# Kernel optimization log

Hardware: AMD Instinct MI355X
Metric: run time of the kernel (lower is better)

Reference implementation:

```python
import jax, jax.numpy as jnp
import numpy as np

B, L, D_IN, D_MODEL, H = 8, 1024, 256, 512, 8
D_HEAD = D_MODEL // H


def setup_inputs() -> dict:
    key = jax.random.key(0)
    ks = jax.random.split(key, 12)
    queries = jax.random.normal(ks[0], (B, L, D_IN), dtype=jnp.float32)
    keys_ = jax.random.normal(ks[1], (B, L, D_IN), dtype=jnp.float32)
    values = jax.random.normal(ks[2], (B, L, D_IN), dtype=jnp.float32)
    attention_mask = jnp.ones((B, L), dtype=jnp.int32)
    # binary symmetric-ish adjacency (sparse molecular graph style)
    adjacency_matrix = (jax.random.uniform(ks[3], (B, L, L)) < 0.05).astype(jnp.float32)
    distance_matrix = jax.random.uniform(ks[4], (B, L, L), dtype=jnp.float32) * 10.0
    s = 1.0 / np.sqrt(D_IN)
    W_q = jax.random.normal(ks[5], (D_MODEL, D_IN), dtype=jnp.float32) * s
    W_k = jax.random.normal(ks[6], (D_MODEL, D_IN), dtype=jnp.float32) * s
    W_v = jax.random.normal(ks[7], (D_MODEL, D_IN), dtype=jnp.float32) * s
    W_o = jax.random.normal(ks[8], (D_MODEL, D_MODEL), dtype=jnp.float32) / np.sqrt(D_MODEL)
    lambda_a = jax.random.normal(ks[9], (H,), dtype=jnp.float32) * 0.1
    lambda_d = jax.random.normal(ks[10], (H,), dtype=jnp.float32) * 0.1
    return {"queries": queries, "keys": keys_, "values": values,
            "attention_mask": attention_mask, "adjacency_matrix": adjacency_matrix,
            "distance_matrix": distance_matrix, "W_q": W_q, "W_k": W_k,
            "W_v": W_v, "W_o": W_o, "lambda_a": lambda_a, "lambda_d": lambda_d}


def _split_heads(x):
    # (b, l, d_model) -> (b, h, l, d_head)
    b, l, _ = x.shape
    return x.reshape(b, l, H, D_HEAD).transpose(0, 2, 1, 3)


def reference(queries, keys, values, attention_mask, adjacency_matrix,
              distance_matrix, W_q, W_k, W_v, W_o, lambda_a, lambda_d):
    Q = _split_heads(queries @ W_q.T)   # (b,h,l,d)
    K = _split_heads(keys @ W_k.T)
    V = _split_heads(values @ W_v.T)
    scores = jnp.einsum("bhqd,bhkd->bhqk", Q, K) / jnp.sqrt(jnp.asarray(D_HEAD, Q.dtype))
    # MSRSA: per-head learned scalars inject graph structure into the scores
    scores = (scores
              + lambda_a[None, :, None, None] * adjacency_matrix[:, None, :, :]
              + lambda_d[None, :, None, None] * distance_matrix[:, None, :, :])
    mask = attention_mask[:, None, None, :] > 0  # (b,1,1,l) key mask
    scores = jnp.where(mask, scores, jnp.asarray(-1e9, scores.dtype))
    attn_weight = jax.nn.softmax(scores, axis=-1)  # (b,h,l,l)
    out = jnp.einsum("bhqk,bhkd->bhqd", attn_weight, V)
    out = out.transpose(0, 2, 1, 3).reshape(queries.shape[0], queries.shape[1], D_MODEL)
    return out @ W_o.T
```

## Files before the change

kernel.cpp:

```cpp
#include <hip/hip_runtime.h>
#include <hip/hip_fp16.h>

#define BB 8
#define LL 1024
#define DIN 256
#define DM 512
#define HH 8
#define DH 64

typedef __attribute__((ext_vector_type(8))) short bf16x8;
typedef __attribute__((ext_vector_type(4))) float f32x4;

__device__ __forceinline__ unsigned short f2bf(float f) {
  union { float f; unsigned u; } c; c.f = f;
  unsigned u = c.u;
  return (unsigned short)((u + 0x7fffu + ((u >> 16) & 1u)) >> 16);
}

#if defined(__has_builtin)
#if __has_builtin(__builtin_amdgcn_cvt_pk_bf16_f32)
#define HAS_PK_BF16 1
#endif
#if __has_builtin(__builtin_amdgcn_fdot2)
#define HAS_FDOT2 1
#endif
#endif

#ifdef HAS_PK_BF16
typedef __bf16 bf2 __attribute__((ext_vector_type(2)));
__device__ __forceinline__ unsigned pk2(float lo, float hi) {
  union { bf2 v; unsigned u; } c;
  c.v = __builtin_amdgcn_cvt_pk_bf16_f32(lo, hi);
  return c.u;
}
#else
__device__ __forceinline__ unsigned pk2(float lo, float hi) {
  return ((unsigned)f2bf(hi) << 16) | f2bf(lo);
}
#endif

typedef _Float16 h2f __attribute__((ext_vector_type(2)));

__device__ __forceinline__ unsigned pkh(float a, float d) {
  return (unsigned)__half_as_ushort(__float2half_rn(a)) |
         ((unsigned)__half_as_ushort(__float2half_rn(d)) << 16);
}

__device__ __forceinline__ void async_copy16(void* lds, const void* g) {
  __builtin_amdgcn_global_load_lds(
      (const __attribute__((address_space(1))) unsigned*)g,
      (__attribute__((address_space(3))) unsigned*)lds, 16, 0, 0);
}

__global__ __launch_bounds__(256) void prep(
    const float* __restrict__ qin, const float* __restrict__ kin,
    const float* __restrict__ vin,
    const float* __restrict__ wq, const float* __restrict__ wk,
    const float* __restrict__ wv, const float* __restrict__ wo,
    const int* __restrict__ msk,
    const float* __restrict__ adj, const float* __restrict__ dis,
    unsigned short* __restrict__ xq, unsigned short* __restrict__ xk,
    unsigned short* __restrict__ xv,
    unsigned short* __restrict__ wqb, unsigned short* __restrict__ wkb,
    unsigned short* __restrict__ wvb, unsigned short* __restrict__ wob,
    float* __restrict__ mad, unsigned* __restrict__ bp)
{
  int t = blockIdx.x * 256 + threadIdx.x;
  const int XS = 524288, WS = 32768;
  if (t < 3 * XS) {
    int seg = t >> 19, off = t & (XS - 1);
    const float* s = (seg == 0) ? qin : (seg == 1) ? kin : vin;
    unsigned short* d = (seg == 0) ? xq : (seg == 1) ? xk : xv;
    float4 f = ((const float4*)s)[off];
    uint2 o = { pk2(f.x, f.y), pk2(f.z, f.w) };
    ((uint2*)d)[off] = o;
    return;
  }
  t -= 3 * XS;
  if (t < 3 * WS) {
    int seg = t >> 15, off = t & (WS - 1);
    const float* s = (seg == 0) ? wq : (seg == 1) ? wk : wv;
    unsigned short* d = (seg == 0) ? wqb : (seg == 1) ? wkb : wvb;
    float4 f = ((const float4*)s)[off];
    uint2 o = { pk2(f.x, f.y), pk2(f.z, f.w) };
    ((uint2*)d)[off] = o;
    return;
  }
  t -= 3 * WS;
  if (t < 65536) {
    float4 f = ((const float4*)wo)[t];
    uint2 o = { pk2(f.x, f.y), pk2(f.z, f.w) };
    ((uint2*)wob)[t] = o;
    return;
  }
  t -= 65536;
  if (t < 2048) {
    int4 m = ((const int4*)msk)[t];
    float4 f = { m.x ? 0.0f : -30000.0f, m.y ? 0.0f : -30000.0f,
                 m.z ? 0.0f : -30000.0f, m.w ? 0.0f : -30000.0f };
    ((float4*)mad)[t] = f;
    return;
  }
  t -= 2048;
  float4 a4 = ((const float4*)adj)[t];
  float4 d4 = ((const float4*)dis)[t];
  uint4 o = { pkh(a4.x, d4.x), pkh(a4.y, d4.y), pkh(a4.z, d4.z), pkh(a4.w, d4.w) };
  ((uint4*)bp)[t] = o;
}

__global__ __launch_bounds__(256) void qkv_proj(
    const unsigned short* __restrict__ xq, const unsigned short* __restrict__ xk,
    const unsigned short* __restrict__ xv,
    const unsigned short* __restrict__ wqb, const unsigned short* __restrict__ wkb,
    const unsigned short* __restrict__ wvb,
    unsigned short* __restrict__ qb, unsigned short* __restrict__ kb,
    unsigned short* __restrict__ vt)
{
  const int t = blockIdx.z;
  const unsigned short* __restrict__ X = (t == 0) ? xq : (t == 1) ? xk : xv;
  const unsigned short* __restrict__ W = (t == 0) ? wqb : (t == 1) ? wkb : wvb;
  const int m0 = blockIdx.y * 128;
  const int h  = blockIdx.x;
  __shared__ __align__(16) char arena[24576];
  const int tid = threadIdx.x;
  const int wid = tid >> 6;
  const int lane = tid & 63;
  const int lo = lane & 15;
  const int quad = lane >> 4;

  f32x4 acc[2][4];
#pragma unroll
  for (int mi = 0; mi < 2; ++mi)
#pragma unroll
    for (int ni = 0; ni < 4; ++ni) acc[mi][ni] = (f32x4)0.0f;

#pragma unroll
  for (int j = 0; j < 2; ++j) {
    int id = j * 256 + tid, r = id >> 2, c = id & 3;
    async_copy16(arena + j * 4096 + wid * 1024,
                 X + (size_t)(m0 + r) * DIN + ((c ^ (r & 3)) * 8));
  }
  {
    int id = tid, r = id >> 2, c = id & 3;
    async_copy16(arena + 16384 + wid * 1024,
                 W + (size_t)(h * 64 + r) * DIN + ((c ^ (r & 3)) * 8));
  }
  __syncthreads();

  for (int it = 0; it < 8; ++it) {
    const int p = it & 1;
    if (it < 7) {
      const int kk = (it + 1) * 32, q = 1 - p;
#pragma unroll
      for (int j = 0; j < 2; ++j) {
        int id = j * 256 + tid, r = id >> 2, c = id & 3;
        async_copy16(arena + q * 8192 + j * 4096 + wid * 1024,
                     X + (size_t)(m0 + r) * DIN + kk + ((c ^ (r & 3)) * 8));
      }
      {
        int id = tid, r = id >> 2, c = id & 3;
        async_copy16(arena + 16384 + q * 4096 + wid * 1024,
                     W + (size_t)(h * 64 + r) * DIN + kk + ((c ^ (r & 3)) * 8));
      }
    }
    const unsigned short* Ab = (const unsigned short*)(arena + p * 8192);
    const unsigned short* Bb = (const unsigned short*)(arena + 16384 + p * 4096);
    bf16x8 a[2], bfr[4];
#pragma unroll
    for (int mi = 0; mi < 2; ++mi) {
      int R = wid * 32 + mi * 16 + lo;
      a[mi] = *(const bf16x8*)&Ab[R * 32 + ((quad ^ (R & 3)) * 8)];
    }
#pragma unroll
    for (int ni = 0; ni < 4; ++ni) {
      int N = ni * 16 + lo;
      bfr[ni] = *(const bf16x8*)&Bb[N * 32 + ((quad ^ (N & 3)) * 8)];
    }
#pragma unroll
    for (int mi = 0; mi < 2; ++mi)
#pragma unroll
      for (int ni = 0; ni < 4; ++ni)
        acc[mi][ni] = __builtin_amdgcn_mfma_f32_16x16x32_bf16(
            a[mi], bfr[ni], acc[mi][ni], 0, 0, 0);
    __syncthreads();
  }

  const int b = m0 >> 10;
  const int lbase0 = (m0 & 1023) + wid * 32;
  if (t < 2) {
    unsigned short* dstp = (t == 0) ? qb : kb;
#pragma unroll
    for (int mi = 0; mi < 2; ++mi)
#pragma unroll
      for (int ni = 0; ni < 4; ++ni) {
        int d = ni * 16 + lo;
#pragma unroll
        for (int r = 0; r < 4; ++r) {
          int lb = lbase0 + mi * 16 + quad * 4 + r;
          dstp[((size_t)(b * HH + h) * LL + lb) * DH + d] = f2bf(acc[mi][ni][r]);
        }
      }
  } else {
#pragma unroll
    for (int mi = 0; mi < 2; ++mi)
#pragma unroll
      for (int ni = 0; ni < 4; ++ni) {
        int d = ni * 16 + lo;
        int lb = lbase0 + mi * 16 + quad * 4;
        uint2 o = { pk2(acc[mi][ni][0], acc[mi][ni][1]),
                    pk2(acc[mi][ni][2], acc[mi][ni][3]) };
        *(uint2*)&vt[((size_t)(b * HH + h) * DH + d) * LL + lb] = o;
      }
  }
}

__global__ __launch_bounds__(256, 4) void attn(
    const unsigned short* __restrict__ qb, const unsigned short* __restrict__ kb,
    const unsigned short* __restrict__ vt,
    const float* __restrict__ mad, const unsigned* __restrict__ bp,
    const float* __restrict__ la_, const float* __restrict__ ld_,
    unsigned short* __restrict__ ao)
{
  const int bi = blockIdx.x;
  const int b  = bi & 7;
  const int hg = (bi >> 3) & 3;
  const int q0 = (bi >> 5) * 32;
  const int tid = threadIdx.x;
  const int wid = tid >> 6;
  const int lane = tid & 63;
  const int lo = lane & 15;
  const int quad = lane >> 4;
  const int h  = hg * 2 + (wid & 1);
  const int kh = wid >> 1;
  const int bh = b * HH + h;

  __shared__ __align__(16) char arena[17408];
  unsigned short* pbufw = (unsigned short*)arena + wid * 1280;
  float*          mgbuf = (float*)arena;

  const float LOG2E = 1.44269504f;
  const float la2 = la_[h] * LOG2E, ld2 = ld_[h] * LOG2E;
  const float sc2 = 0.125f * LOG2E;
#ifdef HAS_FDOT2
  h2f lam2;
  lam2.x = (_Float16)la2;
  lam2.y = (_Float16)ld2;
#endif

  const unsigned short* qp = qb + ((size_t)bh * LL + q0) * DH;
  bf16x8 qB[2][2];
#pragma unroll
  for (int nj = 0; nj < 2; ++nj)
#pragma unroll
    for (int ki = 0; ki < 2; ++ki)
      qB[nj][ki] = *(const bf16x8*)&qp[(nj * 16 + lo) * DH + ki * 32 + quad * 8];

  const unsigned short* kp = kb + (size_t)bh * LL * DH;
  const unsigned short* vp = vt + (size_t)bh * DH * LL;
  const unsigned* bpp = bp + ((size_t)b * LL + q0) * LL;
  const float* mp = mad + b * LL;

  f32x4 o[4][2];
  float rs[2] = {0.0f, 0.0f};
#pragma unroll
  for (int md = 0; md < 4; ++md)
#pragma unroll
    for (int nj = 0; nj < 2; ++nj) o[md][nj] = (f32x4)0.0f;

  const int kbeg = kh * (LL / 2);

  for (int jt = 0; jt < 16; ++jt) {
    const int k0 = kbeg + jt * 32;

    bf16x8 kA[2][2];
#pragma unroll
    for (int mi = 0; mi < 2; ++mi)
#pragma unroll
      for (int ki = 0; ki < 2; ++ki)
        kA[mi][ki] = *(const bf16x8*)&kp[(size_t)(k0 + mi * 16 + lo) * DH +
                                         ki * 32 + quad * 8];
    bf16x8 vA[4];
#pragma unroll
    for (int md = 0; md < 4; ++md)
      vA[md] = *(const bf16x8*)&vp[(md * 16 + lo) * LL + k0 + quad * 8];
    f32x4 msv[2];
#pragma unroll
    for (int mi = 0; mi < 2; ++mi)
      msv[mi] = *(const f32x4*)&mp[k0 + mi * 16 + quad * 4];

    f32x4 s[2][2];
#pragma unroll
    for (int mi = 0; mi < 2; ++mi)
#pragma unroll
      for (int nj = 0; nj < 2; ++nj) s[mi][nj] = (f32x4)0.0f;
#pragma unroll
    for (int ki = 0; ki < 2; ++ki)
#pragma unroll
      for (int mi = 0; mi < 2; ++mi)
#pragma unroll
        for (int nj = 0; nj < 2; ++nj)
          s[mi][nj] = __builtin_amdgcn_mfma_f32_16x16x32_bf16(
              kA[mi][ki], qB[nj][ki], s[mi][nj], 0, 0, 0);

#pragma unroll
    for (int mi = 0; mi < 2; ++mi)
#pragma unroll
      for (int nj = 0; nj < 2; ++nj) {
        uint4 u = *(const uint4*)&bpp[(size_t)(nj * 16 + lo) * LL +
                                      k0 + mi * 16 + quad * 4];
        float p4[4];
#pragma unroll
        for (int r = 0; r < 4; ++r) {
          float t = fmaf(s[mi][nj][r], sc2, msv[mi][r]);
#ifdef HAS_FDOT2
          union { unsigned v; h2f hv; } c; c.v = u[r];
          p4[r] = __builtin_amdgcn_exp2f(
              __builtin_amdgcn_fdot2(c.hv, lam2, t, false));
#else
          union { unsigned v; __half2 hh; } c; c.v = u[r];
          float tt = fmaf(__high2float(c.hh), ld2, t);
          p4[r] = __builtin_amdgcn_exp2f(fmaf(__low2float(c.hh), la2, tt));
#endif
        }
        rs[nj] += (p4[0] + p4[1]) + (p4[2] + p4[3]);
        uint2 w = { pk2(p4[0], p4[1]), pk2(p4[2], p4[3]) };
        *(uint2*)&pbufw[(nj * 16 + lo) * 40 + mi * 16 + quad * 4] = w;
      }

    asm volatile("s_waitcnt lgkmcnt(0)" ::: "memory");

    bf16x8 pB[2];
#pragma unroll
    for (int nj = 0; nj < 2; ++nj)
      pB[nj] = *(const bf16x8*)&pbufw[(nj * 16 + lo) * 40 + quad * 8];

#pragma unroll
    for (int md = 0; md < 4; ++md)
#pragma unroll
      for (int nj = 0; nj < 2; ++nj)
        o[md][nj] = __builtin_amdgcn_mfma_f32_16x16x32_bf16(
            vA[md], pB[nj], o[md][nj], 0, 0, 0);
  }

  __syncthreads();
  const int hs = wid & 1;
  if (kh == 1) {
#pragma unroll
    for (int md = 0; md < 4; ++md)
#pragma unroll
      for (int nj = 0; nj < 2; ++nj)
#pragma unroll
        for (int r = 0; r < 4; ++r)
          mgbuf[hs * 2176 + ((md * 2 + nj) * 4 + r) * 64 + lane] = o[md][nj][r];
    mgbuf[hs * 2176 + 32 * 64 + lane] = rs[0];
    mgbuf[hs * 2176 + 33 * 64 + lane] = rs[1];
  }
  __syncthreads();
  if (kh == 0) {
#pragma unroll
    for (int md = 0; md < 4; ++md)
#pragma unroll
      for (int nj = 0; nj < 2; ++nj)
#pragma unroll
        for (int r = 0; r < 4; ++r)
          o[md][nj][r] += mgbuf[hs * 2176 + ((md * 2 + nj) * 4 + r) * 64 + lane];
    rs[0] += mgbuf[hs * 2176 + 32 * 64 + lane];
    rs[1] += mgbuf[hs * 2176 + 33 * 64 + lane];
    float inv[2];
#pragma unroll
    for (int nj = 0; nj < 2; ++nj) {
      rs[nj] += __shfl_xor(rs[nj], 16);
      rs[nj] += __shfl_xor(rs[nj], 32);
      inv[nj] = __builtin_amdgcn_rcpf(rs[nj]);
    }
#pragma unroll
    for (int md = 0; md < 4; ++md)
#pragma unroll
      for (int nj = 0; nj < 2; ++nj) {
        int l = q0 + nj * 16 + lo;
        uint2 st = { pk2(o[md][nj][0] * inv[nj], o[md][nj][1] * inv[nj]),
                     pk2(o[md][nj][2] * inv[nj], o[md][nj][3] * inv[nj]) };
        *(uint2*)&ao[((size_t)b * LL + l) * DM + h * DH + md * 16 + quad * 4] = st;
      }
  }
}

__global__ __launch_bounds__(256) void oproj(
    const unsigned short* __restrict__ ao, const unsigned short* __restrict__ wob,
    float* __restrict__ out)
{
  const int m0 = blockIdx.y * 128;
  const int n0 = blockIdx.x * 64;
  __shared__ __align__(16) char arena[24576];
  const int tid = threadIdx.x;
  const int wid = tid >> 6;
  const int lane = tid & 63;
  const int lo = lane & 15;
  const int quad = lane >> 4;

  f32x4 acc[2][4];
#pragma unroll
  for (int mi = 0; mi < 2; ++mi)
#pragma unroll
    for (int ni = 0; ni < 4; ++ni) acc[mi][ni] = (f32x4)0.0f;

#pragma unroll
  for (int j = 0; j < 2; ++j) {
    int id = j * 256 + tid, r = id >> 2, c = id & 3;
    async_copy16(arena + j * 4096 + wid * 1024,
                 ao + (size_t)(m0 + r) * DM + ((c ^ (r & 3)) * 8));
  }
  {
    int id = tid, r = id >> 2, c = id & 3;
    async_copy16(arena + 16384 + wid * 1024,
                 wob + (size_t)(n0 + r) * DM + ((c ^ (r & 3)) * 8));
  }
  __syncthreads();

  for (int it = 0; it < 16; ++it) {
    const int p = it & 1;
    if (it < 15) {
      const int kk = (it + 1) * 32, q = 1 - p;
#pragma unroll
      for (int j = 0; j < 2; ++j) {
        int id = j * 256 + tid, r = id >> 2, c = id & 3;
        async_copy16(arena + q * 8192 + j * 4096 + wid * 1024,
                     ao + (size_t)(m0 + r) * DM + kk + ((c ^ (r & 3)) * 8));
      }
      {
        int id = tid, r = id >> 2, c = id & 3;
        async_copy16(arena + 16384 + q * 4096 + wid * 1024,
                     wob + (size_t)(n0 + r) * DM + kk + ((c ^ (r & 3)) * 8));
      }
    }
    const unsigned short* Ab = (const unsigned short*)(arena + p * 8192);
    const unsigned short* Bb = (const unsigned short*)(arena + 16384 + p * 4096);
    bf16x8 a[2], bfr[4];
#pragma unroll
    for (int mi = 0; mi < 2; ++mi) {
      int R = wid * 32 + mi * 16 + lo;
      a[mi] = *(const bf16x8*)&Ab[R * 32 + ((quad ^ (R & 3)) * 8)];
    }
#pragma unroll
    for (int ni = 0; ni < 4; ++ni) {
      int N = ni * 16 + lo;
      bfr[ni] = *(const bf16x8*)&Bb[N * 32 + ((quad ^ (N & 3)) * 8)];
    }
#pragma unroll
    for (int mi = 0; mi < 2; ++mi)
#pragma unroll
      for (int ni = 0; ni < 4; ++ni)
        acc[mi][ni] = __builtin_amdgcn_mfma_f32_16x16x32_bf16(
            a[mi], bfr[ni], acc[mi][ni], 0, 0, 0);
    __syncthreads();
  }

#pragma unroll
  for (int mi = 0; mi < 2; ++mi)
#pragma unroll
    for (int ni = 0; ni < 4; ++ni)
#pragma unroll
      for (int r = 0; r < 4; ++r)
        out[(size_t)(m0 + wid * 32 + mi * 16 + quad * 4 + r) * DM +
            n0 + ni * 16 + lo] = acc[mi][ni][r];
}

extern "C" void kernel_launch(void* const* d_in, const int* in_sizes, int n_in,
                              void* d_out, int out_size, void* d_ws, size_t ws_size,
                              hipStream_t stream) {
  const float* qin = (const float*)d_in[0];
  const float* kin = (const float*)d_in[1];
  const float* vin = (const float*)d_in[2];
  const int*   msk = (const int*)d_in[3];
  const float* adj = (const float*)d_in[4];
  const float* dis = (const float*)d_in[5];
  const float* wq  = (const float*)d_in[6];
  const float* wk  = (const float*)d_in[7];
  const float* wv  = (const float*)d_in[8];
  const float* wo  = (const float*)d_in[9];
  const float* la  = (const float*)d_in[10];
  const float* ld  = (const float*)d_in[11];
  float* out = (float*)d_out;

  const size_t tensb = (size_t)BB * HH * LL * DH;
  const size_t xsz   = (size_t)BB * LL * DIN;
  unsigned short* qb  = (unsigned short*)d_ws;
  unsigned short* kb  = qb + tensb;
  unsigned short* vt  = kb + tensb;
  unsigned short* ao  = vt + tensb;
  unsigned short* xq  = ao;
  unsigned short* xk  = ao + xsz;
  unsigned short* xv  = ao + tensb;
  unsigned short* wqb = xv + xsz;
  unsigned short* wkb = wqb + (size_t)DM * DIN;
  unsigned short* wvb = wkb + (size_t)DM * DIN;
  unsigned short* wob = wvb + (size_t)DM * DIN;
  float*          mdd = (float*)(wob + (size_t)DM * DM);
  unsigned*       bpk = (unsigned*)(mdd + (size_t)BB * LL);

  prep<<<dim3(14984), 256, 0, stream>>>(qin, kin, vin, wq, wk, wv, wo, msk,
                                        adj, dis,
                                        xq, xk, xv, wqb, wkb, wvb, wob, mdd, bpk);
  qkv_proj<<<dim3(8, 64, 3), 256, 0, stream>>>(xq, xk, xv, wqb, wkb, wvb, qb, kb, vt);
  attn<<<dim3(1024), 256, 0, stream>>>(qb, kb, vt, mdd, bpk, la, ld, ao);
  oproj<<<dim3(8, 64), 256, 0, stream>>>(ao, wob, out);
}
```

Baseline: 270.8 us.

## Prefetch next K tile and issue bias loads before score MFMAs in attention loop

Restructures the attention inner loop into a manually double-buffered pair of tiles. The K fragment for the next tile is loaded while the current tile computes, and the packed adjacency/distance bias, mask and V loads are issued up front behind a sched_barrier, so global latency overlaps the score MFMAs. The launch-bounds occupancy hint drops from 4 to 3 blocks to leave room for the extra registers, and the fdot2 bias path becomes unconditional on device. The risks are higher register pressure and lower occupancy.

```diff
diff --git a/kernel.cpp b/kernel.cpp
--- a/kernel.cpp
+++ b/kernel.cpp
@@ -10,6 +10,7 @@
 
 typedef __attribute__((ext_vector_type(8))) short bf16x8;
 typedef __attribute__((ext_vector_type(4))) float f32x4;
+typedef _Float16 h2f __attribute__((ext_vector_type(2)));
 
 __device__ __forceinline__ unsigned short f2bf(float f) {
   union { float f; unsigned u; } c; c.f = f;
@@ -21,12 +22,9 @@
 #if __has_builtin(__builtin_amdgcn_cvt_pk_bf16_f32)
 #define HAS_PK_BF16 1
 #endif
-#if __has_builtin(__builtin_amdgcn_fdot2)
-#define HAS_FDOT2 1
 #endif
-#endif
-
-#ifdef HAS_PK_BF16
+
+#if defined(HAS_PK_BF16)
 typedef __bf16 bf2 __attribute__((ext_vector_type(2)));
 __device__ __forceinline__ unsigned pk2(float lo, float hi) {
   union { bf2 v; unsigned u; } c;
@@ -39,7 +37,15 @@
 }
 #endif
 
-typedef _Float16 h2f __attribute__((ext_vector_type(2)));
+__device__ __forceinline__ float biasdot(unsigned u, h2f lam, float t) {
+#if defined(__HIP_DEVICE_COMPILE__)
+  union { unsigned v; h2f hv; } c; c.v = u;
+  return __builtin_amdgcn_fdot2(c.hv, lam, t, false);
+#else
+  (void)u; (void)lam;
+  return t;
+#endif
+}
 
 __device__ __forceinline__ unsigned pkh(float a, float d) {
   return (unsigned)__half_as_ushort(__float2half_rn(a)) |
@@ -214,7 +220,7 @@
   }
 }
 
-__global__ __launch_bounds__(256, 4) void attn(
+__global__ __launch_bounds__(256, 3) void attn(
     const unsigned short* __restrict__ qb, const unsigned short* __restrict__ kb,
     const unsigned short* __restrict__ vt,
     const float* __restrict__ mad, const unsigned* __restrict__ bp,
@@ -241,11 +247,9 @@
   const float LOG2E = 1.44269504f;
   const float la2 = la_[h] * LOG2E, ld2 = ld_[h] * LOG2E;
   const float sc2 = 0.125f * LOG2E;
-#ifdef HAS_FDOT2
   h2f lam2;
   lam2.x = (_Float16)la2;
   lam2.y = (_Float16)ld2;
-#endif
 
   const unsigned short* qp = qb + ((size_t)bh * LL + q0) * DH;
   bf16x8 qB[2][2];
@@ -269,78 +273,68 @@
 
   const int kbeg = kh * (LL / 2);
 
-  for (int jt = 0; jt < 16; ++jt) {
-    const int k0 = kbeg + jt * 32;
-
-    bf16x8 kA[2][2];
-#pragma unroll
-    for (int mi = 0; mi < 2; ++mi)
-#pragma unroll
-      for (int ki = 0; ki < 2; ++ki)
-        kA[mi][ki] = *(const bf16x8*)&kp[(size_t)(k0 + mi * 16 + lo) * DH +
-                                         ki * 32 + quad * 8];
-    bf16x8 vA[4];
-#pragma unroll
-    for (int md = 0; md < 4; ++md)
-      vA[md] = *(const bf16x8*)&vp[(md * 16 + lo) * LL + k0 + quad * 8];
-    f32x4 msv[2];
-#pragma unroll
-    for (int mi = 0; mi < 2; ++mi)
-      msv[mi] = *(const f32x4*)&mp[k0 + mi * 16 + quad * 4];
-
-    f32x4 s[2][2];
-#pragma unroll
-    for (int mi = 0; mi < 2; ++mi)
-#pragma unroll
-      for (int nj = 0; nj < 2; ++nj) s[mi][nj] = (f32x4)0.0f;
+  bf16x8 kA0[2][2], kA1[2][2];
+#pragma unroll
+  for (int mi = 0; mi < 2; ++mi)
 #pragma unroll
     for (int ki = 0; ki < 2; ++ki)
-#pragma unroll
-      for (int mi = 0; mi < 2; ++mi)
-#pragma unroll
-        for (int nj = 0; nj < 2; ++nj)
-          s[mi][nj] = __builtin_amdgcn_mfma_f32_16x16x32_bf16(
-              kA[mi][ki], qB[nj][ki], s[mi][nj], 0, 0, 0);
-
-#pragma unroll
-    for (int mi = 0; mi < 2; ++mi)
-#pragma unroll
-      for (int nj = 0; nj < 2; ++nj) {
-        uint4 u = *(const uint4*)&bpp[(size_t)(nj * 16 + lo) * LL +
-                                      k0 + mi * 16 + quad * 4];
-        float p4[4];
-#pragma unroll
-        for (int r = 0; r < 4; ++r) {
-          float t = fmaf(s[mi][nj][r], sc2, msv[mi][r]);
-#ifdef HAS_FDOT2
-          union { unsigned v; h2f hv; } c; c.v = u[r];
-          p4[r] = __builtin_amdgcn_exp2f(
-              __builtin_amdgcn_fdot2(c.hv, lam2, t, false));
-#else
-          union { unsigned v; __half2 hh; } c; c.v = u[r];
-          float tt = fmaf(__high2float(c.hh), ld2, t);
-          p4[r] = __builtin_amdgcn_exp2f(fmaf(__low2float(c.hh), la2, tt));
-#endif
-        }
-        rs[nj] += (p4[0] + p4[1]) + (p4[2] + p4[3]);
-        uint2 w = { pk2(p4[0], p4[1]), pk2(p4[2], p4[3]) };
-        *(uint2*)&pbufw[(nj * 16 + lo) * 40 + mi * 16 + quad * 4] = w;
-      }
-
-    asm volatile("s_waitcnt lgkmcnt(0)" ::: "memory");
-
-    bf16x8 pB[2];
-#pragma unroll
-    for (int nj = 0; nj < 2; ++nj)
-      pB[nj] = *(const bf16x8*)&pbufw[(nj * 16 + lo) * 40 + quad * 8];
-
-#pragma unroll
-    for (int md = 0; md < 4; ++md)
-#pragma unroll
-      for (int nj = 0; nj < 2; ++nj)
-        o[md][nj] = __builtin_amdgcn_mfma_f32_16x16x32_bf16(
-            vA[md], pB[nj], o[md][nj], 0, 0, 0);
-  }
+      kA0[mi][ki] = *(const bf16x8*)&kp[(size_t)(kbeg + mi * 16 + lo) * DH +
+                                        ki * 32 + quad * 8];
+
+#define ATTN_TILE(KC, KN, JT)                                                  \
+  do {                                                                         \
+    const int k0 = kbeg + (JT) * 32;                                           \
+    const int kn0 = ((JT) < 15) ? (k0 + 32) : k0;   \
+    uint4 ub[2][2];                                                            \
+    _Pragma("unroll") for (int mi = 0; mi < 2; ++mi)                           \
+      _Pragma("unroll") for (int nj = 0; nj < 2; ++nj)                         \
+        ub[mi][nj] = *(const uint4*)&bpp[(size_t)(nj * 16 + lo) * LL +         \
+                                         k0 + mi * 16 + quad * 4];             \
+    f32x4 msv[2];                                                              \
+    _Pragma("unroll") for (int mi = 0; mi < 2; ++mi)                           \
+      msv[mi] = *(const f32x4*)&mp[k0 + mi * 16 + quad * 4];                   \
+    bf16x8 vA[4];                                                              \
+    _Pragma("unroll") for (int md = 0; md < 4; ++md)                           \
+      vA[md] = *(const bf16x8*)&vp[(md * 16 + lo) * LL + k0 + quad * 8];       \
+    _Pragma("unroll") for (int mi = 0; mi < 2; ++mi)                           \
+      _Pragma("unroll") for (int ki = 0; ki < 2; ++ki)                         \
+        KN[mi][ki] = *(const bf16x8*)&kp[(size_t)(kn0 + mi * 16 + lo) * DH +   \
+                                         ki * 32 + quad * 8];                  \
+    __builtin_amdgcn_sched_barrier(0);           \
+    f32x4 s[2][2];                                                             \
+    _Pragma("unroll") for (int mi = 0; mi < 2; ++mi)                           \
+      _Pragma("unroll") for (int nj = 0; nj < 2; ++nj) s[mi][nj] = (f32x4)0.0f;\
+    _Pragma("unroll") for (int ki = 0; ki < 2; ++ki)                           \
+      _Pragma("unroll") for (int mi = 0; mi < 2; ++mi)                         \
+        _Pragma("unroll") for (int nj = 0; nj < 2; ++nj)                       \
+          s[mi][nj] = __builtin_amdgcn_mfma_f32_16x16x32_bf16(                 \
+              KC[mi][ki], qB[nj][ki], s[mi][nj], 0, 0, 0);                     \
+    _Pragma("unroll") for (int mi = 0; mi < 2; ++mi)                           \
+      _Pragma("unroll") for (int nj = 0; nj < 2; ++nj) {                       \
+        float p4[4];                                                           \
+        _Pragma("unroll") for (int r = 0; r < 4; ++r) {                        \
+          float tb = fmaf(s[mi][nj][r], sc2, msv[mi][r]);                      \
+          p4[r] = __builtin_amdgcn_exp2f(biasdot(ub[mi][nj][r], lam2, tb));    \
+        }                                                                      \
+        rs[nj] += (p4[0] + p4[1]) + (p4[2] + p4[3]);                           \
+        uint2 w = { pk2(p4[0], p4[1]), pk2(p4[2], p4[3]) };                    \
+        *(uint2*)&pbufw[(nj * 16 + lo) * 40 + mi * 16 + quad * 4] = w;         \
+      }                                                                        \
+    asm volatile("s_waitcnt lgkmcnt(0)" ::: "memory");                         \
+    bf16x8 pB[2];                                                              \
+    _Pragma("unroll") for (int nj = 0; nj < 2; ++nj)                           \
+      pB[nj] = *(const bf16x8*)&pbufw[(nj * 16 + lo) * 40 + quad * 8];         \
+    _Pragma("unroll") for (int md = 0; md < 4; ++md)                           \
+      _Pragma("unroll") for (int nj = 0; nj < 2; ++nj)                         \
+        o[md][nj] = __builtin_amdgcn_mfma_f32_16x16x32_bf16(                   \
+            vA[md], pB[nj], o[md][nj], 0, 0, 0);                               \
+  } while (0)
+
+  for (int j2 = 0; j2 < 8; ++j2) {
+    ATTN_TILE(kA0, kA1, 2 * j2);
+    ATTN_TILE(kA1, kA0, 2 * j2 + 1);
+  }
+#undef ATTN_TILE
 
   __syncthreads();
   const int hs = wid & 1;
```

New measurement: 276.7 us. 1.02x slower.
